# Performance work log

Measured on AMD Instinct MI355X. Metric: run time of the kernel, lower is better.

The kernel has to match this reference:

```python
import jax, jax.numpy as jnp
import numpy as np

EPS = 1e-5

@jax.custom_vjp
def spike(u):
    return (u >= 0).astype(u.dtype)

def _spike_fwd(u):
    return spike(u), u

def _spike_bwd(u, g):
    return (g / (1.0 + 5.0 * jnp.abs(u)) ** 2,)

spike.defvjp(_spike_fwd, _spike_bwd)


def setup_inputs() -> dict:
    key = jax.random.key(0)
    ks = jax.random.split(key, 20)
    B, T, IN, TH, H = 2048, 320, 64, 128, 64
    d = {}
    d['x'] = jax.random.normal(ks[0], (B, T, IN), jnp.float32)
    d['tda'] = jax.random.normal(ks[1], (B, 150), jnp.float32)
    # depthwise conv: Conv1d(64,128,k=15,pad=7,groups=64) -> kernel [128, 1, 15]
    d['conv_w'] = jax.random.normal(ks[2], (TH, 1, 15), jnp.float32) * 0.1
    d['conv_b'] = jnp.zeros((TH,), jnp.float32)
    d['bn1_g'] = jnp.ones((TH,), jnp.float32)
    d['bn1_b'] = jnp.zeros((TH,), jnp.float32)
    d['bn1_m'] = jnp.zeros((TH,), jnp.float32)
    d['bn1_v'] = jnp.ones((TH,), jnp.float32)
    # spatial_fc: Linear(128,64), init mean=0.05 std=0.1
    d['sp_w'] = 0.05 + 0.1 * jax.random.normal(ks[3], (H, TH), jnp.float32)
    d['sp_b'] = jnp.zeros((H,), jnp.float32)
    d['li_w'] = jax.random.normal(ks[4], (H, 2 * H), jnp.float32) * (1.0 / np.sqrt(2 * H))
    d['li_b'] = jnp.zeros((H,), jnp.float32)
    d['tda_w1'] = jax.random.normal(ks[5], (64, 150), jnp.float32) * (1.0 / np.sqrt(150))
    d['tda_b1'] = jnp.zeros((64,), jnp.float32)
    d['tda_w2'] = jax.random.normal(ks[6], (32, 64), jnp.float32) * 0.125
    d['tda_b2'] = jnp.zeros((32,), jnp.float32)
    dp_out = (320 // 32) * H  # 640
    d['cls_w1'] = jax.random.normal(ks[7], (128, dp_out + 32), jnp.float32) * (1.0 / np.sqrt(dp_out + 32))
    d['cls_b1'] = jnp.zeros((128,), jnp.float32)
    d['bn2_g'] = jnp.ones((128,), jnp.float32)
    d['bn2_b'] = jnp.zeros((128,), jnp.float32)
    d['bn2_m'] = jnp.zeros((128,), jnp.float32)
    d['bn2_v'] = jnp.ones((128,), jnp.float32)
    d['cls_w2'] = jax.random.normal(ks[8], (4, 128), jnp.float32) * (1.0 / np.sqrt(128))
    d['cls_b2'] = jnp.zeros((4,), jnp.float32)
    return d


def reference(x, tda, conv_w, conv_b, bn1_g, bn1_b, bn1_m, bn1_v, sp_w, sp_b,
              li_w, li_b, tda_w1, tda_b1, tda_w2, tda_b2,
              cls_w1, cls_b1, bn2_g, bn2_b, bn2_m, bn2_v, cls_w2, cls_b2):
    B, T, _ = x.shape
    L_DP, N_DP, H = 32, 16, 64
    # temp_conv (eval mode: no dropout, BN with running stats)
    xc = jnp.transpose(x, (0, 2, 1))  # [B, 64, T]
    y = jax.lax.conv_general_dilated(
        xc, conv_w, window_strides=(1,), padding=[(7, 7)],
        dimension_numbers=('NCH', 'OIH', 'NCH'), feature_group_count=64)
    y = y + conv_b[None, :, None]
    y = (y - bn1_m[None, :, None]) * jax.lax.rsqrt(bn1_v + EPS)[None, :, None] * bn1_g[None, :, None] + bn1_b[None, :, None]
    y = jax.nn.relu(y)
    y = jnp.transpose(y, (0, 2, 1))  # [B, T, 128]
    # precompute all input currents: [T, B, 64] (time-major for scan)
    cur_all = jnp.einsum('bth,oh->tbo', y, sp_w) + sp_b

    def step(carry, cur):
        mf, ms, ml = carry
        mf = 0.5 * mf + cur
        sf = spike(mf - 0.5)
        mf = mf * (1.0 - sf)
        ms = 0.9 * ms + cur
        ss = spike(ms - 1.0)
        ms = ms * (1.0 - ss)
        cur_li = jnp.concatenate([sf, ss], axis=-1) @ li_w.T + li_b
        ml = 0.9 * ml + cur_li
        return (mf, ms, ml), ml

    z0 = jnp.zeros((B, H), x.dtype)
    _, li_seq = jax.lax.scan(step, (z0, z0, z0), cur_all)  # [T, B, 64]
    li_seq = jnp.transpose(li_seq, (1, 0, 2))  # [B, T, 64]

    windows = li_seq.reshape(B, T // L_DP, L_DP, H)
    start_mean = windows[:, :, :N_DP, :].mean(axis=2)
    end_mean = windows[:, :, -N_DP:, :].mean(axis=2)
    dp_feat = (end_mean - start_mean).reshape(B, -1)  # [B, 640]

    t1 = jax.nn.relu(tda @ tda_w1.T + tda_b1)
    tda_feat = jax.nn.relu(t1 @ tda_w2.T + tda_b2)  # [B, 32]

    h = jnp.concatenate([dp_feat, tda_feat], axis=-1) @ cls_w1.T + cls_b1
    h = (h - bn2_m) * jax.lax.rsqrt(bn2_v + EPS) * bn2_g + bn2_b
    h = jax.nn.relu(h)
    return h @ cls_w2.T + cls_b2  # [B, 4]
```

## Files before the change

kernel.cpp:

```cpp
#include <hip/hip_runtime.h>

#define NT 256

#define WS_SPWT    0
#define WS_SC1     8192
#define WS_SH1     8320
#define WS_SC2     8448
#define WS_SH2     8576
#define WS_LIWT    8704
#define WS_TW1T    16896
#define WS_TW2T    26496
#define WS_CW1T    28544
#define WS_TOTAL   114560
#define WS_WG      114560
#define WS_WBASE   114688
#define WS_CURBASE (114688 + 2048*1280)
#define CUR_STRIDE 20480

__global__ void prep_kernel(
    const float* __restrict__ conv_b, const float* __restrict__ bn1_g,
    const float* __restrict__ bn1_b,  const float* __restrict__ bn1_m,
    const float* __restrict__ bn1_v,  const float* __restrict__ sp_w,
    const float* __restrict__ li_w,   const float* __restrict__ tda_w1,
    const float* __restrict__ tda_w2, const float* __restrict__ cls_w1,
    const float* __restrict__ bn2_g,  const float* __restrict__ bn2_b,
    const float* __restrict__ bn2_m,  const float* __restrict__ bn2_v,
    float* __restrict__ ws)
{
    int i = blockIdx.x * NT + threadIdx.x;
    if (i > WS_TOTAL) return;
    if (i == WS_TOTAL) {
        float g = 0.f, sE = 0.f, sL = 0.f; int w = 0;
        for (int t = 0; t < 320; ++t) {
            g = fmaf(0.9f, g, 1.f);
            int pos = t & 31;
            if (pos < 16) sE += g; else sL += g;
            if (pos == 31) { ws[WS_WG + w] = sL - sE; ++w; sE = 0.f; sL = 0.f; }
        }
        return;
    }
    if (i < WS_SC1) {
        int c = i >> 6, h = i & 63;
        ws[i] = sp_w[h*128 + c];
    } else if (i < WS_SH1) {
        int c = i - WS_SC1;
        float vv = bn1_v[c] + 1e-5f;
        ws[i] = (float)((double)bn1_g[c] / sqrt((double)vv));
    } else if (i < WS_SC2) {
        int c = i - WS_SH1;
        float vv = bn1_v[c] + 1e-5f;
        double s = (double)bn1_g[c] / sqrt((double)vv);
        ws[i] = (float)(((double)conv_b[c] - (double)bn1_m[c])*s + (double)bn1_b[c]);
    } else if (i < WS_SH2) {
        int c = i - WS_SC2;
        float vv = bn2_v[c] + 1e-5f;
        ws[i] = (float)((double)bn2_g[c] / sqrt((double)vv));
    } else if (i < WS_LIWT) {
        int c = i - WS_SH2;
        float vv = bn2_v[c] + 1e-5f;
        double s = (double)bn2_g[c] / sqrt((double)vv);
        ws[i] = (float)((double)bn2_b[c] - (double)bn2_m[c]*s);
    } else if (i < WS_TW1T) {
        int t = i - WS_LIWT; int j = t >> 6, o = t & 63;
        ws[i] = li_w[o*128 + j];
    } else if (i < WS_TW2T) {
        int t = i - WS_TW1T; int r = t >> 6, o = t & 63;
        ws[i] = tda_w1[o*150 + r];
    } else if (i < WS_CW1T) {
        int t = i - WS_TW2T; int j = t >> 5, o = t & 31;
        ws[i] = tda_w2[o*64 + j];
    } else {
        int t = i - WS_CW1T; int j = t >> 7, c = t & 127;
        ws[i] = cls_w1[c*672 + j];
    }
}

__launch_bounds__(NT, 4)
__global__ void convproj_kernel(
    const float* __restrict__ x, const float* __restrict__ conv_w,
    const float* __restrict__ ws, float* __restrict__ cur, int b0)
{
    __shared__ float y_lds[128*65];

    const int tid = threadIdx.x;
    const int bi  = blockIdx.x / 5;
    const int chk = blockIdx.x % 5;
    const int t0  = chk * 64;
    const int ic  = tid & 63;
    const int tg  = tid >> 6;

    float w0[15], w1[15];
    #pragma unroll
    for (int k = 0; k < 15; ++k) {
        w0[k] = conv_w[(2*ic)*15 + k];
        w1[k] = conv_w[(2*ic + 1)*15 + k];
    }
    const float sA = ws[WS_SC1 + 2*ic],     hA = ws[WS_SH1 + 2*ic];
    const float sB = ws[WS_SC1 + 2*ic + 1], hB = ws[WS_SH1 + 2*ic + 1];

    const float* xb = x + (size_t)(b0 + bi) * 20480 + ic;
    float xr[30];
    #pragma unroll
    for (int r = 0; r < 30; ++r) {
        int t = t0 + tg*16 - 7 + r;
        xr[r] = ((unsigned)t < 320u) ? xb[(size_t)t * 64] : 0.f;
    }

    #pragma unroll
    for (int j = 0; j < 16; ++j) {
        float a0 = 0.f, a1 = 0.f;
        #pragma unroll
        for (int k = 0; k < 15; ++k) {
            a0 = fmaf(xr[j + k], w0[k], a0);
            a1 = fmaf(xr[j + k], w1[k], a1);
        }
        int tt = tg*16 + j;
        y_lds[(2*ic)*65 + tt]     = fmaxf(fmaf(a0, sA, hA), 0.f);
        y_lds[(2*ic + 1)*65 + tt] = fmaxf(fmaf(a1, sB, hB), 0.f);
    }
    __syncthreads();

    {
        const int lane = tid & 63;
        const int h0 = __builtin_amdgcn_readfirstlane((tid >> 6) << 4);
        const float* __restrict__ spwT = ws;

        float acc[16];
        #pragma unroll
        for (int j = 0; j < 16; ++j) acc[j] = 0.f;
        #pragma unroll 4
        for (int c = 0; c < 128; ++c) {
            float yv = y_lds[c*65 + lane];
            const float4* wp = reinterpret_cast<const float4*>(spwT + c*64 + h0);
            float4 q0 = wp[0], q1 = wp[1], q2 = wp[2], q3 = wp[3];
            acc[0]  = fmaf(yv, q0.x, acc[0]);
            acc[1]  = fmaf(yv, q0.y, acc[1]);
            acc[2]  = fmaf(yv, q0.z, acc[2]);
            acc[3]  = fmaf(yv, q0.w, acc[3]);
            acc[4]  = fmaf(yv, q1.x, acc[4]);
            acc[5]  = fmaf(yv, q1.y, acc[5]);
            acc[6]  = fmaf(yv, q1.z, acc[6]);
            acc[7]  = fmaf(yv, q1.w, acc[7]);
            acc[8]  = fmaf(yv, q2.x, acc[8]);
            acc[9]  = fmaf(yv, q2.y, acc[9]);
            acc[10] = fmaf(yv, q2.z, acc[10]);
            acc[11] = fmaf(yv, q2.w, acc[11]);
            acc[12] = fmaf(yv, q3.x, acc[12]);
            acc[13] = fmaf(yv, q3.y, acc[13]);
            acc[14] = fmaf(yv, q3.z, acc[14]);
            acc[15] = fmaf(yv, q3.w, acc[15]);
        }
        float* cb = cur + (size_t)bi * CUR_STRIDE + (size_t)h0 * 320 + t0 + lane;
        #pragma unroll
        for (int j = 0; j < 16; ++j)
            cb[(size_t)j*320] = acc[j];
    }
}

__device__ __forceinline__ void lif16(float4 n0, float4 n1, float4 n2, float4 n3,
    float spb, float& mf, float& ms, float& rlo, float& rhi,
    float& slo, float& shi)
{
    float v[16] = {n0.x,n0.y,n0.z,n0.w, n1.x,n1.y,n1.z,n1.w,
                   n2.x,n2.y,n2.z,n2.w, n3.x,n3.y,n3.z,n3.w};
    slo = 0.f; shi = 0.f;
    #pragma unroll
    for (int q = 0; q < 16; ++q) {
        float c = v[q] + spb;
        mf = fmaf(0.5f, mf, c);
        bool sf = (mf - 0.5f) >= 0.f;
        ms = fmaf(0.9f, ms, c);
        bool ss = (ms - 1.0f) >= 0.f;
        mf = sf ? 0.f : mf;
        ms = ss ? 0.f : ms;
        rlo = fmaf(0.9f, rlo, sf ? 1.f : 0.f);
        rhi = fmaf(0.9f, rhi, ss ? 1.f : 0.f);
        slo += rlo; shi += rhi;
    }
}

__global__ void scan_kernel(const float* __restrict__ cur,
                            const float* __restrict__ sp_b,
                            float* __restrict__ W, int b0, int nb)
{
    const int wv = (int)((blockIdx.x * (unsigned)blockDim.x + threadIdx.x) >> 6);
    if (wv >= nb) return;
    const int lane = threadIdx.x & 63;
    const float* cb = cur + (size_t)wv * CUR_STRIDE + (size_t)lane * 320;
    const float spb = sp_b[lane];
    float* Wb = W + (size_t)(b0 + wv) * 1280;

    float mf = 0.f, ms = 0.f, rlo = 0.f, rhi = 0.f;

    float4 A0 = *reinterpret_cast<const float4*>(cb);
    float4 A1 = *reinterpret_cast<const float4*>(cb + 4);
    float4 A2 = *reinterpret_cast<const float4*>(cb + 8);
    float4 A3 = *reinterpret_cast<const float4*>(cb + 12);
    float4 B0 = *reinterpret_cast<const float4*>(cb + 16);
    float4 B1 = *reinterpret_cast<const float4*>(cb + 20);
    float4 B2 = *reinterpret_cast<const float4*>(cb + 24);
    float4 B3 = *reinterpret_cast<const float4*>(cb + 28);

    #pragma unroll 1
    for (int tb = 0; tb < 20; tb += 2) {
        float sE_lo, sE_hi, slo, shi;
        lif16(A0, A1, A2, A3, spb, mf, ms, rlo, rhi, sE_lo, sE_hi);
        if (tb + 2 < 20) {
            const float* p = cb + (tb + 2) * 16;
            A0 = *reinterpret_cast<const float4*>(p);
            A1 = *reinterpret_cast<const float4*>(p + 4);
            A2 = *reinterpret_cast<const float4*>(p + 8);
            A3 = *reinterpret_cast<const float4*>(p + 12);
        }
        lif16(B0, B1, B2, B3, spb, mf, ms, rlo, rhi, slo, shi);
        if (tb + 3 < 20) {
            const float* p = cb + (tb + 3) * 16;
            B0 = *reinterpret_cast<const float4*>(p);
            B1 = *reinterpret_cast<const float4*>(p + 4);
            B2 = *reinterpret_cast<const float4*>(p + 8);
            B3 = *reinterpret_cast<const float4*>(p + 12);
        }
        int wdx = tb >> 1;
        Wb[wdx*128 + lane]      = slo - sE_lo;
        Wb[wdx*128 + 64 + lane] = shi - sE_hi;
    }
}

__global__ void epilogue_kernel(
    const float* __restrict__ tda,    const float* __restrict__ li_b,
    const float* __restrict__ tda_b1, const float* __restrict__ tda_b2,
    const float* __restrict__ cls_b1, const float* __restrict__ cls_w2,
    const float* __restrict__ cls_b2, const float* __restrict__ ws,
    const float* __restrict__ W,      float* __restrict__ out)
{
    __shared__ float Wl[1280];
    __shared__ float t1[64], tf[32], dp[640], h1[128];
    const int b = blockIdx.x, tid = threadIdx.x;

    for (int i = tid; i < 1280; i += NT)
        Wl[i] = W[(size_t)b*1280 + i];
    __syncthreads();

    const float* __restrict__ liwT = ws + WS_LIWT;
    const float* __restrict__ tw1T = ws + WS_TW1T;
    const float* __restrict__ tw2T = ws + WS_TW2T;
    const float* __restrict__ cw1T = ws + WS_CW1T;
    const float* tdab = tda + b*150;

    if (tid < 64) {
        float acc = tda_b1[tid];
        for (int i2 = 0; i2 < 150; ++i2)
            acc = fmaf(tdab[i2], tw1T[i2*64 + tid], acc);
        t1[tid] = fmaxf(acc, 0.f);
    }
    __syncthreads();
    if (tid < 32) {
        float acc = tda_b2[tid];
        #pragma unroll 8
        for (int j = 0; j < 64; ++j)
            acc = fmaf(t1[j], tw2T[j*32 + tid], acc);
        tf[tid] = fmaxf(acc, 0.f);
    }
    {
        int o = tid & 63;
        for (int w = tid >> 6; w < 10; w += 4) {
            float acc = li_b[o] * ws[WS_WG + w];
            #pragma unroll 4
            for (int j = 0; j < 128; ++j)
                acc = fmaf(Wl[w*128 + j], liwT[j*64 + o], acc);
            dp[w*64 + o] = 0.0625f * acc;
        }
    }
    __syncthreads();
    if (tid < 128) {
        float acc = cls_b1[tid];
        for (int j = 0; j < 640; ++j)
            acc = fmaf(dp[j], cw1T[j*128 + tid], acc);
        #pragma unroll 4
        for (int j = 0; j < 32; ++j)
            acc = fmaf(tf[j], cw1T[(640 + j)*128 + tid], acc);
        float s2 = ws[WS_SC2 + tid], sh2 = ws[WS_SH2 + tid];
        h1[tid] = fmaxf(fmaf(acc, s2, sh2), 0.f);
    }
    __syncthreads();
    if (tid < 4) {
        float acc = cls_b2[tid];
        for (int c = 0; c < 128; ++c)
            acc = fmaf(h1[c], cls_w2[tid*128 + c], acc);
        out[b*4 + tid] = acc;
    }
}

extern "C" void kernel_launch(void* const* d_in, const int* in_sizes, int n_in,
                              void* d_out, int out_size, void* d_ws, size_t ws_size,
                              hipStream_t stream) {
    const float* x      = (const float*)d_in[0];
    const float* tda    = (const float*)d_in[1];
    const float* conv_w = (const float*)d_in[2];
    const float* conv_b = (const float*)d_in[3];
    const float* bn1_g  = (const float*)d_in[4];
    const float* bn1_b  = (const float*)d_in[5];
    const float* bn1_m  = (const float*)d_in[6];
    const float* bn1_v  = (const float*)d_in[7];
    const float* sp_w   = (const float*)d_in[8];
    const float* sp_b   = (const float*)d_in[9];
    const float* li_w   = (const float*)d_in[10];
    const float* li_b   = (const float*)d_in[11];
    const float* tda_w1 = (const float*)d_in[12];
    const float* tda_b1 = (const float*)d_in[13];
    const float* tda_w2 = (const float*)d_in[14];
    const float* tda_b2 = (const float*)d_in[15];
    const float* cls_w1 = (const float*)d_in[16];
    const float* cls_b1 = (const float*)d_in[17];
    const float* bn2_g  = (const float*)d_in[18];
    const float* bn2_b  = (const float*)d_in[19];
    const float* bn2_m  = (const float*)d_in[20];
    const float* bn2_v  = (const float*)d_in[21];
    const float* cls_w2 = (const float*)d_in[22];
    const float* cls_b2 = (const float*)d_in[23];
    float* ws  = (float*)d_ws;
    float* out = (float*)d_out;

    const int B = in_sizes[0] / (320 * 64);

    prep_kernel<<<(WS_TOTAL + 1 + NT - 1)/NT, NT, 0, stream>>>(
        conv_b, bn1_g, bn1_b, bn1_m, bn1_v, sp_w,
        li_w, tda_w1, tda_w2, cls_w1,
        bn2_g, bn2_b, bn2_m, bn2_v, ws);

    long cap = (long)(ws_size / 4) - (long)WS_CURBASE;
    int nbg = (int)(cap / CUR_STRIDE);
    if (nbg < 1) nbg = 1;
    if (nbg > B) nbg = B;

    for (int g0 = 0; g0 < B; g0 += nbg) {
        int nb = (B - g0 < nbg) ? (B - g0) : nbg;
        convproj_kernel<<<nb*5, NT, 0, stream>>>(
            x, conv_w, ws, ws + WS_CURBASE, g0);
        scan_kernel<<<(nb + 3)/4, NT, 0, stream>>>(
            ws + WS_CURBASE, sp_b, ws + WS_WBASE, g0, nb);
    }

    epilogue_kernel<<<B, NT, 0, stream>>>(
        tda, li_b, tda_b1, tda_b2, cls_b1, cls_w2, cls_b2,
        ws, ws + WS_WBASE, out);
}
```

Baseline: 282.6 us.

## Loop time chunks inside one convproj block per batch and prefetch next chunk

Each convproj block now handles all five 64-step time chunks of one batch element instead of one chunk per block, so there are one fifth as many blocks. While the projection for the current chunk runs, the input rows for the next chunk are loaded into a double-buffered register array. The sp_b bias moves from the scan's inner loop into the projection accumulator's initial value, and the spike comparisons are simplified. In exchange the grid has fewer blocks, which can reduce parallelism and occupancy, and the doubled register arrays and extra barriers add cost.

Result: slower. 289.9 us, median of 2 (+2.6%).

```diff
diff --git a/kernel.cpp b/kernel.cpp
--- a/kernel.cpp
+++ b/kernel.cpp
@@ -78,16 +78,17 @@
 __launch_bounds__(NT, 4)
 __global__ void convproj_kernel(
     const float* __restrict__ x, const float* __restrict__ conv_w,
-    const float* __restrict__ ws, float* __restrict__ cur, int b0)
+    const float* __restrict__ sp_b, const float* __restrict__ ws,
+    float* __restrict__ cur, int b0)
 {
     __shared__ float y_lds[128*65];
 
     const int tid = threadIdx.x;
-    const int bi  = blockIdx.x / 5;
-    const int chk = blockIdx.x % 5;
-    const int t0  = chk * 64;
+    const int bi  = blockIdx.x;
     const int ic  = tid & 63;
     const int tg  = tid >> 6;
+    const int lane = tid & 63;
+    const int h0 = __builtin_amdgcn_readfirstlane((tid >> 6) << 4);
 
     float w0[15], w1[15];
     #pragma unroll
@@ -97,68 +98,94 @@
     }
     const float sA = ws[WS_SC1 + 2*ic],     hA = ws[WS_SH1 + 2*ic];
     const float sB = ws[WS_SC1 + 2*ic + 1], hB = ws[WS_SH1 + 2*ic + 1];
-
+    const float4* bp = reinterpret_cast<const float4*>(sp_b + h0);
+    const float4 b0v = bp[0], b1v = bp[1], b2v = bp[2], b3v = bp[3];
+
+    const float* __restrict__ spwT = ws;
     const float* xb = x + (size_t)(b0 + bi) * 20480 + ic;
-    float xr[30];
+    float* curb = cur + (size_t)bi * CUR_STRIDE;
+
+    float xr0[30], xr1[30];
     #pragma unroll
     for (int r = 0; r < 30; ++r) {
-        int t = t0 + tg*16 - 7 + r;
-        xr[r] = ((unsigned)t < 320u) ? xb[(size_t)t * 64] : 0.f;
+        int t = tg*16 - 7 + r;
+        xr0[r] = (t >= 0) ? xb[(size_t)t * 64] : 0.f;
     }
 
     #pragma unroll
-    for (int j = 0; j < 16; ++j) {
-        float a0 = 0.f, a1 = 0.f;
+    for (int chk = 0; chk < 5; ++chk) {
+        float* xc = (chk & 1) ? xr1 : xr0;
+        float* xn = (chk & 1) ? xr0 : xr1;
+
         #pragma unroll
-        for (int k = 0; k < 15; ++k) {
-            a0 = fmaf(xr[j + k], w0[k], a0);
-            a1 = fmaf(xr[j + k], w1[k], a1);
-        }
-        int tt = tg*16 + j;
-        y_lds[(2*ic)*65 + tt]     = fmaxf(fmaf(a0, sA, hA), 0.f);
-        y_lds[(2*ic + 1)*65 + tt] = fmaxf(fmaf(a1, sB, hB), 0.f);
-    }
-    __syncthreads();
-
-    {
-        const int lane = tid & 63;
-        const int h0 = __builtin_amdgcn_readfirstlane((tid >> 6) << 4);
-        const float* __restrict__ spwT = ws;
-
-        float acc[16];
-        #pragma unroll
-        for (int j = 0; j < 16; ++j) acc[j] = 0.f;
-        #pragma unroll 4
-        for (int c = 0; c < 128; ++c) {
-            float yv = y_lds[c*65 + lane];
-            const float4* wp = reinterpret_cast<const float4*>(spwT + c*64 + h0);
-            float4 q0 = wp[0], q1 = wp[1], q2 = wp[2], q3 = wp[3];
-            acc[0]  = fmaf(yv, q0.x, acc[0]);
-            acc[1]  = fmaf(yv, q0.y, acc[1]);
-            acc[2]  = fmaf(yv, q0.z, acc[2]);
-            acc[3]  = fmaf(yv, q0.w, acc[3]);
-            acc[4]  = fmaf(yv, q1.x, acc[4]);
-            acc[5]  = fmaf(yv, q1.y, acc[5]);
-            acc[6]  = fmaf(yv, q1.z, acc[6]);
-            acc[7]  = fmaf(yv, q1.w, acc[7]);
-            acc[8]  = fmaf(yv, q2.x, acc[8]);
-            acc[9]  = fmaf(yv, q2.y, acc[9]);
-            acc[10] = fmaf(yv, q2.z, acc[10]);
-            acc[11] = fmaf(yv, q2.w, acc[11]);
-            acc[12] = fmaf(yv, q3.x, acc[12]);
-            acc[13] = fmaf(yv, q3.y, acc[13]);
-            acc[14] = fmaf(yv, q3.z, acc[14]);
-            acc[15] = fmaf(yv, q3.w, acc[15]);
-        }
-        float* cb = cur + (size_t)bi * CUR_STRIDE + (size_t)h0 * 320 + t0 + lane;
-        #pragma unroll
-        for (int j = 0; j < 16; ++j)
-            cb[(size_t)j*320] = acc[j];
+        for (int j = 0; j < 16; ++j) {
+            float a0 = 0.f, a1 = 0.f;
+            #pragma unroll
+            for (int k = 0; k < 15; ++k) {
+                a0 = fmaf(xc[j + k], w0[k], a0);
+                a1 = fmaf(xc[j + k], w1[k], a1);
+            }
+            int tt = tg*16 + j;
+            y_lds[(2*ic)*65 + tt]     = fmaxf(fmaf(a0, sA, hA), 0.f);
+            y_lds[(2*ic + 1)*65 + tt] = fmaxf(fmaf(a1, sB, hB), 0.f);
+        }
+        __syncthreads();
+
+        if (chk < 4) {
+            const int tbase = (chk + 1)*64 + tg*16 - 7;
+            if (tbase + 29 < 320) {
+                #pragma unroll
+                for (int r = 0; r < 30; ++r)
+                    xn[r] = xb[(size_t)(tbase + r) * 64];
+            } else {
+                #pragma unroll
+                for (int r = 0; r < 30; ++r) {
+                    int t = tbase + r;
+                    xn[r] = (t < 320) ? xb[(size_t)t * 64] : 0.f;
+                }
+            }
+        }
+
+        {
+            float acc[16];
+            acc[0]=b0v.x;  acc[1]=b0v.y;  acc[2]=b0v.z;  acc[3]=b0v.w;
+            acc[4]=b1v.x;  acc[5]=b1v.y;  acc[6]=b1v.z;  acc[7]=b1v.w;
+            acc[8]=b2v.x;  acc[9]=b2v.y;  acc[10]=b2v.z; acc[11]=b2v.w;
+            acc[12]=b3v.x; acc[13]=b3v.y; acc[14]=b3v.z; acc[15]=b3v.w;
+
+            #pragma unroll 4
+            for (int c = 0; c < 128; ++c) {
+                float yv = y_lds[c*65 + lane];
+                const float4* wp = reinterpret_cast<const float4*>(spwT + c*64 + h0);
+                float4 q0 = wp[0], q1 = wp[1], q2 = wp[2], q3 = wp[3];
+                acc[0]  = fmaf(yv, q0.x, acc[0]);
+                acc[1]  = fmaf(yv, q0.y, acc[1]);
+                acc[2]  = fmaf(yv, q0.z, acc[2]);
+                acc[3]  = fmaf(yv, q0.w, acc[3]);
+                acc[4]  = fmaf(yv, q1.x, acc[4]);
+                acc[5]  = fmaf(yv, q1.y, acc[5]);
+                acc[6]  = fmaf(yv, q1.z, acc[6]);
+                acc[7]  = fmaf(yv, q1.w, acc[7]);
+                acc[8]  = fmaf(yv, q2.x, acc[8]);
+                acc[9]  = fmaf(yv, q2.y, acc[9]);
+                acc[10] = fmaf(yv, q2.z, acc[10]);
+                acc[11] = fmaf(yv, q2.w, acc[11]);
+                acc[12] = fmaf(yv, q3.x, acc[12]);
+                acc[13] = fmaf(yv, q3.y, acc[13]);
+                acc[14] = fmaf(yv, q3.z, acc[14]);
+                acc[15] = fmaf(yv, q3.w, acc[15]);
+            }
+            float* cb = curb + (size_t)h0 * 320 + chk*64 + lane;
+            #pragma unroll
+            for (int j = 0; j < 16; ++j)
+                cb[(size_t)j*320] = acc[j];
+        }
+        __syncthreads();
     }
 }
 
 __device__ __forceinline__ void lif16(float4 n0, float4 n1, float4 n2, float4 n3,
-    float spb, float& mf, float& ms, float& rlo, float& rhi,
+    float& mf, float& ms, float& rlo, float& rhi,
     float& slo, float& shi)
 {
     float v[16] = {n0.x,n0.y,n0.z,n0.w, n1.x,n1.y,n1.z,n1.w,
@@ -166,11 +193,11 @@
     slo = 0.f; shi = 0.f;
     #pragma unroll
     for (int q = 0; q < 16; ++q) {
-        float c = v[q] + spb;
+        float c = v[q];
         mf = fmaf(0.5f, mf, c);
-        bool sf = (mf - 0.5f) >= 0.f;
+        bool sf = mf >= 0.5f;
         ms = fmaf(0.9f, ms, c);
-        bool ss = (ms - 1.0f) >= 0.f;
+        bool ss = ms >= 1.0f;
         mf = sf ? 0.f : mf;
         ms = ss ? 0.f : ms;
         rlo = fmaf(0.9f, rlo, sf ? 1.f : 0.f);
@@ -180,14 +207,12 @@
 }
 
 __global__ void scan_kernel(const float* __restrict__ cur,
-                            const float* __restrict__ sp_b,
                             float* __restrict__ W, int b0, int nb)
 {
     const int wv = (int)((blockIdx.x * (unsigned)blockDim.x + threadIdx.x) >> 6);
     if (wv >= nb) return;
     const int lane = threadIdx.x & 63;
     const float* cb = cur + (size_t)wv * CUR_STRIDE + (size_t)lane * 320;
-    const float spb = sp_b[lane];
     float* Wb = W + (size_t)(b0 + wv) * 1280;
 
     float mf = 0.f, ms = 0.f, rlo = 0.f, rhi = 0.f;
@@ -204,7 +229,7 @@
     #pragma unroll 1
     for (int tb = 0; tb < 20; tb += 2) {
         float sE_lo, sE_hi, slo, shi;
-        lif16(A0, A1, A2, A3, spb, mf, ms, rlo, rhi, sE_lo, sE_hi);
+        lif16(A0, A1, A2, A3, mf, ms, rlo, rhi, sE_lo, sE_hi);
         if (tb + 2 < 20) {
             const float* p = cb + (tb + 2) * 16;
             A0 = *reinterpret_cast<const float4*>(p);
@@ -212,7 +237,7 @@
             A2 = *reinterpret_cast<const float4*>(p + 8);
             A3 = *reinterpret_cast<const float4*>(p + 12);
         }
-        lif16(B0, B1, B2, B3, spb, mf, ms, rlo, rhi, slo, shi);
+        lif16(B0, B1, B2, B3, mf, ms, rlo, rhi, slo, shi);
         if (tb + 3 < 20) {
             const float* p = cb + (tb + 3) * 16;
             B0 = *reinterpret_cast<const float4*>(p);
@@ -335,10 +360,10 @@
 
     for (int g0 = 0; g0 < B; g0 += nbg) {
         int nb = (B - g0 < nbg) ? (B - g0) : nbg;
-        convproj_kernel<<<nb*5, NT, 0, stream>>>(
-            x, conv_w, ws, ws + WS_CURBASE, g0);
+        convproj_kernel<<<nb, NT, 0, stream>>>(
+            x, conv_w, sp_b, ws, ws + WS_CURBASE, g0);
         scan_kernel<<<(nb + 3)/4, NT, 0, stream>>>(
-            ws + WS_CURBASE, sp_b, ws + WS_WBASE, g0, nb);
+            ws + WS_CURBASE, ws + WS_WBASE, g0, nb);
     }
 
     epilogue_kernel<<<B, NT, 0, stream>>>(
```
